# Optimization experiments

Hardware: AMD Instinct MI355X
Metric: run time of the kernel (lower is better)

Reference implementation:

```python
import jax, jax.numpy as jnp
import numpy as np

NUM_GROUPS = 32
EPS = 1e-5


def group_norm(x, scale, bias):
    # x: [B, C, H, W]
    B, C, H, W = x.shape
    g = x.reshape(B, NUM_GROUPS, C // NUM_GROUPS * H * W)
    mean = g.mean(axis=-1, keepdims=True)
    var = g.var(axis=-1, keepdims=True)
    g = (g - mean) * jax.lax.rsqrt(var + EPS)
    g = g.reshape(B, C, H, W)
    return g * scale[None, :, None, None] + bias[None, :, None, None]


def conv1x1(x, w, b):
    # x: [B, C, H, W], w: [O, C], b: [O]
    return jnp.einsum('bchw,oc->bohw', x, w) + b[None, :, None, None]


def setup_inputs() -> dict:
    key = jax.random.key(0)
    ks = jax.random.split(key, 11)
    B, C, H, W = 32, 256, 32, 32
    s = 1.0 / np.sqrt(C)
    return {
        'x': jax.random.normal(ks[0], (B, C, H, W), jnp.float32),
        'gn_scale': jnp.ones((C,), jnp.float32),
        'gn_bias': jnp.zeros((C,), jnp.float32),
        'wq': jax.random.normal(ks[1], (C, C), jnp.float32) * s,
        'bq': jnp.zeros((C,), jnp.float32),
        'wk': jax.random.normal(ks[2], (C, C), jnp.float32) * s,
        'bk': jnp.zeros((C,), jnp.float32),
        'wv': jax.random.normal(ks[3], (C, C), jnp.float32) * s,
        'bv': jnp.zeros((C,), jnp.float32),
        'wo': jax.random.normal(ks[4], (C, C), jnp.float32) * s,
        'bo': jnp.zeros((C,), jnp.float32),
    }


def reference(x, gn_scale, gn_bias, wq, bq, wk, bk, wv, bv, wo, bo):
    B, C, H, W = x.shape
    h = group_norm(x, gn_scale, gn_bias)
    q = conv1x1(h, wq, bq).reshape(B, C, H * W)  # [B, C, N]
    k = conv1x1(h, wk, bk).reshape(B, C, H * W)
    v = conv1x1(h, wv, bv).reshape(B, C, H * W)
    # scores: [B, N, N]
    w = jnp.einsum('bcn,bcm->bnm', q, k) * (C ** -0.5)
    w = jax.nn.softmax(w, axis=-1)
    o = jnp.einsum('bnm,bcm->bcn', w, v).reshape(B, C, H, W)
    o = conv1x1(o, wo, bo)
    return x + o
```

## Files before the change

kernel.cpp:

```cpp
#include <hip/hip_runtime.h>

typedef __attribute__((ext_vector_type(4))) float f32x4;
typedef __attribute__((ext_vector_type(16))) float f32x16;
typedef __attribute__((ext_vector_type(8))) short bf16x8;

__device__ __forceinline__ unsigned short f2bf(float f) {
  union { float f; unsigned u; } v; v.f = f;
  unsigned r = (v.u + 0x7FFFu + ((v.u >> 16) & 1u)) >> 16;
  return (unsigned short)r;
}

__device__ __forceinline__ unsigned cvt_pk_bf16(float lo, float hi) {
  unsigned r;
  asm("v_cvt_pk_bf16_f32 %0, %1, %2" : "=v"(r) : "v"(lo), "v"(hi));
  return r;
}

__device__ __forceinline__ void load16_lds(const void* g, void* l) {
  __builtin_amdgcn_global_load_lds(
      (__attribute__((address_space(1))) void*)(uintptr_t)g,
      (__attribute__((address_space(3))) void*)(unsigned int)(uintptr_t)l,
      16, 0, 0);
}

#define QSCALE 0.09016844f

__global__ __launch_bounds__(256) void convert_w(
    const float* __restrict__ wq, const float* __restrict__ wk,
    const float* __restrict__ wv, const float* __restrict__ wo,
    const float* __restrict__ bq, const float* __restrict__ bk,
    unsigned short* __restrict__ wqkb, unsigned short* __restrict__ wvb,
    unsigned short* __restrict__ wob, float* __restrict__ bqkf) {
  const float* src[4] = {wq, wk, wv, wo};
  unsigned short* dst[4] = {wqkb, wqkb + 65536, wvb, wob};
  int ti = blockIdx.y;
  float sc = (ti == 0) ? QSCALE : 1.f;
  int idx = blockIdx.x * 256 + threadIdx.x;
  float4 v = ((const float4*)src[ti])[idx];
  ushort4 r;
  r.x = f2bf(v.x * sc); r.y = f2bf(v.y * sc);
  r.z = f2bf(v.z * sc); r.w = f2bf(v.w * sc);
  ((ushort4*)dst[ti])[idx] = r;
  if (ti == 3 && blockIdx.x == 0) {
    bqkf[threadIdx.x] = bq[threadIdx.x] * QSCALE;
    bqkf[256 + threadIdx.x] = bk[threadIdx.x];
  }
}

__global__ __launch_bounds__(256) void gn_kernel(
    const float* __restrict__ x, const float* __restrict__ gamma,
    const float* __restrict__ beta, unsigned short* __restrict__ h) {
  __shared__ float xs[8 * 1024];
  __shared__ float red[16];
  const int t = threadIdx.x;
  const int b = blockIdx.x >> 5, g = blockIdx.x & 31;
  const float* xp = x + (size_t)(b * 256 + g * 8) * 1024;
  float s = 0.f, ss = 0.f;
#pragma unroll
  for (int j = 0; j < 8; ++j) {
    float4 v = ((const float4*)xp)[j * 256 + t];
    ((float4*)xs)[j * 256 + t] = v;
    s += v.x + v.y + v.z + v.w;
    ss += v.x * v.x + v.y * v.y + v.z * v.z + v.w * v.w;
  }
#pragma unroll
  for (int o = 32; o >= 1; o >>= 1) {
    s += __shfl_xor(s, o);
    ss += __shfl_xor(ss, o);
  }
  const int wave = t >> 6, lane = t & 63;
  if (lane == 0) { red[wave] = s; red[wave + 4] = ss; }
  __syncthreads();
  s = red[0] + red[1] + red[2] + red[3];
  ss = red[4] + red[5] + red[6] + red[7];
  float mean = s * (1.f / 8192.f);
  float var = ss * (1.f / 8192.f) - mean * mean;
  float rstd = rsqrtf(var + 1e-5f);
  float a[8], c[8];
#pragma unroll
  for (int ci = 0; ci < 8; ++ci) {
    float gm = gamma[g * 8 + ci], bt = beta[g * 8 + ci];
    a[ci] = rstd * gm;
    c[ci] = bt - mean * rstd * gm;
  }
  unsigned short* hb = h + (size_t)b * 1024 * 256 + g * 8;
#pragma unroll
  for (int j = 0; j < 4; ++j) {
    int n = j * 256 + t;
    float f0 = xs[0 * 1024 + n] * a[0] + c[0];
    float f1 = xs[1 * 1024 + n] * a[1] + c[1];
    float f2 = xs[2 * 1024 + n] * a[2] + c[2];
    float f3 = xs[3 * 1024 + n] * a[3] + c[3];
    float f4 = xs[4 * 1024 + n] * a[4] + c[4];
    float f5 = xs[5 * 1024 + n] * a[5] + c[5];
    float f6 = xs[6 * 1024 + n] * a[6] + c[6];
    float f7 = xs[7 * 1024 + n] * a[7] + c[7];
    uint4 o4;
    o4.x = (unsigned)f2bf(f0) | ((unsigned)f2bf(f1) << 16);
    o4.y = (unsigned)f2bf(f2) | ((unsigned)f2bf(f3) << 16);
    o4.z = (unsigned)f2bf(f4) | ((unsigned)f2bf(f5) << 16);
    o4.w = (unsigned)f2bf(f6) | ((unsigned)f2bf(f7) << 16);
    *(uint4*)(hb + (size_t)n * 256) = o4;
  }
}

template <bool OUT_F32, int BIAS_MODE, bool HAS_RES>
__global__ __launch_bounds__(256) void gemm_bt(
    const unsigned short* __restrict__ A, long long sAb,
    const unsigned short* __restrict__ Bm, long long sBb,
    void* __restrict__ Cv, long long sCb,
    const float* __restrict__ bias,
    const float* __restrict__ res, long long sRb,
    int M, int N, int K, float alpha) {
  __shared__ unsigned short As[128 * 32];
  __shared__ unsigned short Bs[128 * 32];
  const int t = threadIdx.x;
  const int wave = t >> 6, lane = t & 63;
  const int bm = blockIdx.y * 128, bn = blockIdx.x * 128;
  const int bz = blockIdx.z;
  const unsigned short* Ab = A + (size_t)bz * sAb;
  const unsigned short* Bb = Bm + (size_t)bz * sBb;
  const int wm = (wave >> 1) * 64, wn = (wave & 1) * 64;
  const int srow = t >> 2;
  const int schunk = t & 3;
  const int lrow = lane & 15, kg = lane >> 4;

  f32x4 acc[4][4] = {};

  for (int k0 = 0; k0 < K; k0 += 32) {
#pragma unroll
    for (int r = 0; r < 2; ++r) {
      int row = r * 64 + srow;
      int cs = schunk ^ ((row >> 1) & 3);
      const unsigned short* ga = Ab + (size_t)(bm + row) * K + (k0 + cs * 8);
      const unsigned short* gb = Bb + (size_t)(bn + row) * K + (k0 + cs * 8);
      load16_lds(ga, &As[(r * 64 + wave * 16) * 32]);
      load16_lds(gb, &Bs[(r * 64 + wave * 16) * 32]);
    }
    __syncthreads();
    bf16x8 af[4], bfr[4];
#pragma unroll
    for (int i = 0; i < 4; ++i) {
      int ra = wm + i * 16 + lrow;
      af[i] = *(const bf16x8*)&As[ra * 32 + ((kg ^ ((ra >> 1) & 3)) * 8)];
      int rb = wn + i * 16 + lrow;
      bfr[i] = *(const bf16x8*)&Bs[rb * 32 + ((kg ^ ((rb >> 1) & 3)) * 8)];
    }
#pragma unroll
    for (int i = 0; i < 4; ++i)
#pragma unroll
      for (int j = 0; j < 4; ++j)
        acc[i][j] = __builtin_amdgcn_mfma_f32_16x16x32_bf16(af[i], bfr[j], acc[i][j], 0, 0, 0);
    __syncthreads();
  }

#pragma unroll
  for (int i = 0; i < 4; ++i) {
#pragma unroll
    for (int j = 0; j < 4; ++j) {
#pragma unroll
      for (int r = 0; r < 4; ++r) {
        int m = bm + wm + i * 16 + (lane >> 4) * 4 + r;
        int n = bn + wn + j * 16 + lrow;
        float v = acc[i][j][r] * alpha;
        if constexpr (BIAS_MODE == 1) v += bias[m];
        if constexpr (BIAS_MODE == 2) v += bias[n];
        if constexpr (HAS_RES) v += res[(size_t)bz * sRb + (size_t)m * N + n];
        if constexpr (OUT_F32)
          ((float*)Cv)[(size_t)bz * sCb + (size_t)m * N + n] = v;
        else
          ((unsigned short*)Cv)[(size_t)bz * sCb + (size_t)m * N + n] = f2bf(v);
      }
    }
  }
}

__global__ __launch_bounds__(512, 2) void flash_attn(
    const unsigned short* __restrict__ qk,
    const unsigned short* __restrict__ vt,
    unsigned short* __restrict__ ot) {
  __shared__ unsigned short SMEM[81920];
  const int VS = 32768, PB = 65536;

  const int t = threadIdx.x;
  const int wave = t >> 6, lane = t & 63;
  const int wr = wave >> 1, wh = wave & 1;
  const int lrow = lane & 15, hi = lane >> 4;
  const int l31 = lane & 31, h2 = lane >> 5;

  const int lbid = blockIdx.x;
  const int logical = (lbid & 7) * 32 + (lbid >> 3);
  const int b = logical >> 3;
  const int q0 = (logical & 7) * 128;

  const unsigned short* qb = qk + (size_t)b * 1024 * 512;
  const unsigned short* kb = qb + 256;
  const unsigned short* vb = vt + (size_t)b * 1024 * 256;

#pragma unroll
  for (int p = 0; p < 4; ++p) {
    int row = p * 16 + wave * 2 + (lane >> 5);
    int ch = l31 ^ (row & 31);
    load16_lds(kb + (size_t)row * 512 + ch * 8, &SMEM[(p * 16 + wave * 2) * 256]);
  }

  bf16x8 aq[16];
#pragma unroll
  for (int kk = 0; kk < 16; ++kk)
    aq[kk] = *(const bf16x8*)(qb + (size_t)(q0 + wr * 32 + l31) * 512 + kk * 16 + h2 * 8);

  f32x4 acco[2][8] = {};
  float lsum = 0.f;

  asm volatile("s_waitcnt vmcnt(0)" ::: "memory");
  __builtin_amdgcn_s_barrier();
  __builtin_amdgcn_sched_barrier(0);

  for (int tt = 0; tt <= 16; ++tt) {
    const int cur = tt & 1, nxt = cur ^ 1;

    if (tt < 15) {
      const unsigned short* kn = kb + (size_t)(tt + 1) * 64 * 512;
#pragma unroll
      for (int p = 0; p < 4; ++p) {
        int row = p * 16 + wave * 2 + (lane >> 5);
        int ch = l31 ^ (row & 31);
        load16_lds(kn + (size_t)row * 512 + ch * 8, &SMEM[nxt * 16384 + (p * 16 + wave * 2) * 256]);
      }
    }
    if (tt < 16) {
      const unsigned short* vn = vb + tt * 64;
#pragma unroll
      for (int p = 0; p < 4; ++p) {
        int row = p * 64 + wave * 8 + (lane >> 3);
        int ch = (lane & 7) ^ (row & 7);
        load16_lds(vn + (size_t)row * 1024 + ch * 8, &SMEM[VS + cur * 16384 + (p * 64 + wave * 8) * 64]);
      }
    }

    f32x16 accs = {};
    if (tt < 16) {
      const int kbase = cur * 16384;
      const int krow = (wh * 32 + l31) * 256;
      __builtin_amdgcn_s_setprio(1);
#pragma unroll
      for (int kk = 0; kk < 16; ++kk) {
        bf16x8 kf = *(const bf16x8*)&SMEM[kbase + krow + (((kk * 2 + h2) ^ l31) << 3)];
        accs = __builtin_amdgcn_mfma_f32_32x32x16_bf16(kf, aq[kk], accs, 0, 0, 0);
      }
      __builtin_amdgcn_s_setprio(0);
    }

    if (tt >= 1) {
      const unsigned short* Pp = &SMEM[PB + nxt * 8192];
      const unsigned short* Vp = &SMEM[VS + nxt * 16384];
#pragma unroll
      for (int kk2 = 0; kk2 < 2; ++kk2) {
        int qa0 = wr * 32 + lrow;
        int qa1 = qa0 + 16;
        bf16x8 pa0 = *(const bf16x8*)&Pp[qa0 * 64 + ((kk2 * 32 + hi * 8) ^ ((qa0 & 7) << 3))];
        bf16x8 pa1 = *(const bf16x8*)&Pp[qa1 * 64 + ((kk2 * 32 + hi * 8) ^ ((qa1 & 7) << 3))];
        __builtin_amdgcn_s_setprio(1);
#pragma unroll
        for (int jj = 0; jj < 8; ++jj) {
          int c = wh * 128 + jj * 16 + lrow;
          bf16x8 bv8 = *(const bf16x8*)&Vp[c * 64 + (((kk2 * 4 + hi) ^ (c & 7)) * 8)];
          acco[0][jj] = __builtin_amdgcn_mfma_f32_16x16x32_bf16(pa0, bv8, acco[0][jj], 0, 0, 0);
          acco[1][jj] = __builtin_amdgcn_mfma_f32_16x16x32_bf16(pa1, bv8, acco[1][jj], 0, 0, 0);
        }
        __builtin_amdgcn_s_setprio(0);
      }
    }

    if (tt < 16) {
      char* Pw = (char*)&SMEM[PB + cur * 8192];
      const int q = wr * 32 + l31;
      const int qoff = q * 128 + (h2 << 3);
      const int qx = (q & 7);
#pragma unroll
      for (int m = 0; m < 4; ++m) {
        float e0 = __builtin_amdgcn_exp2f(accs[4 * m + 0]);
        float e1 = __builtin_amdgcn_exp2f(accs[4 * m + 1]);
        float e2 = __builtin_amdgcn_exp2f(accs[4 * m + 2]);
        float e3 = __builtin_amdgcn_exp2f(accs[4 * m + 3]);
        lsum += (e0 + e1) + (e2 + e3);
        uint2 w2;
        w2.x = cvt_pk_bf16(e0, e1);
        w2.y = cvt_pk_bf16(e2, e3);
        int c = wh * 4 + m;
        *(uint2*)(Pw + qoff + ((c ^ qx) << 4)) = w2;
      }
    }

    asm volatile("s_waitcnt vmcnt(0) lgkmcnt(0)" ::: "memory");
    __builtin_amdgcn_s_barrier();
    __builtin_amdgcn_sched_barrier(0);
  }

  lsum += __shfl_xor(lsum, 32);
  float* lred = (float*)SMEM;
  if (lane < 32) lred[wave * 32 + lane] = lsum;
  __syncthreads();

  unsigned short* ob = ot + (size_t)b * 1024 * 256;
#pragma unroll
  for (int i = 0; i < 2; ++i) {
    float inv[4];
#pragma unroll
    for (int r = 0; r < 4; ++r) {
      int rl = wr * 32 + i * 16 + hi * 4 + r;
      inv[r] = 1.f / (lred[wr * 64 + (rl & 31)] + lred[wr * 64 + 32 + (rl & 31)]);
    }
#pragma unroll
    for (int jj = 0; jj < 8; ++jj)
#pragma unroll
      for (int r = 0; r < 4; ++r) {
        int n = q0 + wr * 32 + i * 16 + hi * 4 + r;
        int c = wh * 128 + jj * 16 + lrow;
        ob[(size_t)n * 256 + c] = f2bf(acco[i][jj][r] * inv[r]);
      }
  }
}

extern "C" void kernel_launch(void* const* d_in, const int* in_sizes, int n_in,
                              void* d_out, int out_size, void* d_ws, size_t ws_size,
                              hipStream_t stream) {
  const float* x    = (const float*)d_in[0];
  const float* gnsc = (const float*)d_in[1];
  const float* gnb  = (const float*)d_in[2];
  const float* wq   = (const float*)d_in[3];
  const float* bq   = (const float*)d_in[4];
  const float* wk   = (const float*)d_in[5];
  const float* bk   = (const float*)d_in[6];
  const float* wv   = (const float*)d_in[7];
  const float* bv   = (const float*)d_in[8];
  const float* wo   = (const float*)d_in[9];
  const float* bo   = (const float*)d_in[10];
  float* out = (float*)d_out;

  unsigned short* wqkb = (unsigned short*)d_ws;
  unsigned short* wvb  = wqkb + 131072;
  unsigned short* wob  = wvb + 65536;
  float*          bqkf = (float*)(wob + 65536);
  unsigned short* h    = wob + 65536 + 2048;
  unsigned short* qkb  = h + 8388608;
  unsigned short* vt   = qkb + 16777216;
  unsigned short* ot   = h;

  const long long sHN = 1024LL * 256;
  const long long sQK = 1024LL * 512;

  convert_w<<<dim3(64, 4), 256, 0, stream>>>(wq, wk, wv, wo, bq, bk, wqkb, wvb, wob, bqkf);
  gn_kernel<<<dim3(1024), 256, 0, stream>>>(x, gnsc, gnb, h);
  gemm_bt<false, 2, false><<<dim3(4, 8, 32), 256, 0, stream>>>(
      h, sHN, wqkb, 0, qkb, sQK, bqkf, nullptr, 0, 1024, 512, 256, 1.f);
  gemm_bt<false, 1, false><<<dim3(8, 2, 32), 256, 0, stream>>>(
      wvb, 0, h, sHN, vt, sHN, bv, nullptr, 0, 256, 1024, 256, 1.f);
  flash_attn<<<dim3(256), 512, 0, stream>>>(qkb, vt, ot);
  gemm_bt<true, 1, true><<<dim3(8, 2, 32), 256, 0, stream>>>(
      wob, 0, ot, sHN, out, sHN, bo, x, sHN, 256, 1024, 256, 1.f);
}
```

Baseline: 118.7 us.

## Merge weight conversion into GN, fuse QK/V projections, double-buffer GEMM, reswizzle P

Folds the weight-conversion kernel into the group-norm launch as 16 extra blocks, and merges the QK and V projection GEMMs into one launch. This removes two kernel launches. The GEMM core now double-buffers its LDS tiles so the next K-slice load overlaps the MFMAs, and it raises wave priority around the MFMA block. The attention kernel's P-tile swizzle gains a row-dependent rotation to reduce LDS bank conflicts. The trade-off is twice the LDS per GEMM block and a runtime bias-mode branch in the epilogue.

Result: no change. 118.2 us (-0.4%).

```diff
diff --git a/kernel.cpp b/kernel.cpp
--- a/kernel.cpp
+++ b/kernel.cpp
@@ -25,34 +25,42 @@
 
 #define QSCALE 0.09016844f
 
-__global__ __launch_bounds__(256) void convert_w(
+__global__ __launch_bounds__(256) void gn_conv_kernel(
+    const float* __restrict__ x, const float* __restrict__ gamma,
+    const float* __restrict__ beta, unsigned short* __restrict__ h,
     const float* __restrict__ wq, const float* __restrict__ wk,
     const float* __restrict__ wv, const float* __restrict__ wo,
     const float* __restrict__ bq, const float* __restrict__ bk,
     unsigned short* __restrict__ wqkb, unsigned short* __restrict__ wvb,
     unsigned short* __restrict__ wob, float* __restrict__ bqkf) {
-  const float* src[4] = {wq, wk, wv, wo};
-  unsigned short* dst[4] = {wqkb, wqkb + 65536, wvb, wob};
-  int ti = blockIdx.y;
-  float sc = (ti == 0) ? QSCALE : 1.f;
-  int idx = blockIdx.x * 256 + threadIdx.x;
-  float4 v = ((const float4*)src[ti])[idx];
-  ushort4 r;
-  r.x = f2bf(v.x * sc); r.y = f2bf(v.y * sc);
-  r.z = f2bf(v.z * sc); r.w = f2bf(v.w * sc);
-  ((ushort4*)dst[ti])[idx] = r;
-  if (ti == 3 && blockIdx.x == 0) {
-    bqkf[threadIdx.x] = bq[threadIdx.x] * QSCALE;
-    bqkf[256 + threadIdx.x] = bk[threadIdx.x];
-  }
-}
-
-__global__ __launch_bounds__(256) void gn_kernel(
-    const float* __restrict__ x, const float* __restrict__ gamma,
-    const float* __restrict__ beta, unsigned short* __restrict__ h) {
   __shared__ float xs[8 * 1024];
   __shared__ float red[16];
   const int t = threadIdx.x;
+
+  if (blockIdx.x >= 1024) {
+    const int wblk = blockIdx.x - 1024;
+    const float* src[4] = {wq, wk, wv, wo};
+    unsigned short* dst[4] = {wqkb, wqkb + 65536, wvb, wob};
+    const int ti = wblk >> 2, part = wblk & 3;
+    const float sc = (ti == 0) ? QSCALE : 1.f;
+    const float* s = src[ti];
+    unsigned short* d = dst[ti];
+#pragma unroll
+    for (int j = 0; j < 16; ++j) {
+      int idx = part * 4096 + j * 256 + t;
+      float4 v = ((const float4*)s)[idx];
+      ushort4 r;
+      r.x = f2bf(v.x * sc); r.y = f2bf(v.y * sc);
+      r.z = f2bf(v.z * sc); r.w = f2bf(v.w * sc);
+      ((ushort4*)d)[idx] = r;
+    }
+    if (wblk == 0) {
+      bqkf[t] = bq[t] * QSCALE;
+      bqkf[256 + t] = bk[t];
+    }
+    return;
+  }
+
   const int b = blockIdx.x >> 5, g = blockIdx.x & 31;
   const float* xp = x + (size_t)(b * 256 + g * 8) * 1024;
   float s = 0.f, ss = 0.f;
@@ -104,54 +112,64 @@
   }
 }
 
-template <bool OUT_F32, int BIAS_MODE, bool HAS_RES>
-__global__ __launch_bounds__(256) void gemm_bt(
-    const unsigned short* __restrict__ A, long long sAb,
-    const unsigned short* __restrict__ Bm, long long sBb,
-    void* __restrict__ Cv, long long sCb,
-    const float* __restrict__ bias,
-    const float* __restrict__ res, long long sRb,
-    int M, int N, int K, float alpha) {
-  __shared__ unsigned short As[128 * 32];
-  __shared__ unsigned short Bs[128 * 32];
+template <bool OUT_F32, bool HAS_RES>
+__device__ __forceinline__ void gemm_core(
+    const unsigned short* __restrict__ Ab, const unsigned short* __restrict__ Bb,
+    void* __restrict__ Cb, const float* __restrict__ bias, int bias_mode,
+    const float* __restrict__ res, int bm, int bn, int N, int K,
+    unsigned short* As, unsigned short* Bs) {
   const int t = threadIdx.x;
   const int wave = t >> 6, lane = t & 63;
-  const int bm = blockIdx.y * 128, bn = blockIdx.x * 128;
-  const int bz = blockIdx.z;
-  const unsigned short* Ab = A + (size_t)bz * sAb;
-  const unsigned short* Bb = Bm + (size_t)bz * sBb;
   const int wm = (wave >> 1) * 64, wn = (wave & 1) * 64;
-  const int srow = t >> 2;
-  const int schunk = t & 3;
+  const int srow = t >> 2, schunk = t & 3;
   const int lrow = lane & 15, kg = lane >> 4;
 
   f32x4 acc[4][4] = {};
 
-  for (int k0 = 0; k0 < K; k0 += 32) {
-#pragma unroll
-    for (int r = 0; r < 2; ++r) {
-      int row = r * 64 + srow;
-      int cs = schunk ^ ((row >> 1) & 3);
-      const unsigned short* ga = Ab + (size_t)(bm + row) * K + (k0 + cs * 8);
-      const unsigned short* gb = Bb + (size_t)(bn + row) * K + (k0 + cs * 8);
-      load16_lds(ga, &As[(r * 64 + wave * 16) * 32]);
-      load16_lds(gb, &Bs[(r * 64 + wave * 16) * 32]);
-    }
-    __syncthreads();
+#pragma unroll
+  for (int r = 0; r < 2; ++r) {
+    int row = r * 64 + srow;
+    int cs = schunk ^ ((row >> 1) & 3);
+    load16_lds(Ab + (size_t)(bm + row) * K + cs * 8, &As[(r * 64 + wave * 16) * 32]);
+    load16_lds(Bb + (size_t)(bn + row) * K + cs * 8, &Bs[(r * 64 + wave * 16) * 32]);
+  }
+  asm volatile("s_waitcnt vmcnt(0)" ::: "memory");
+  __builtin_amdgcn_s_barrier();
+  __builtin_amdgcn_sched_barrier(0);
+
+  const int nk = K >> 5;
+  for (int kt = 0; kt < nk; ++kt) {
+    const int cur = kt & 1;
+    if (kt + 1 < nk) {
+      const int k0 = (kt + 1) << 5;
+      const int boff = (cur ^ 1) * 4096;
+#pragma unroll
+      for (int r = 0; r < 2; ++r) {
+        int row = r * 64 + srow;
+        int cs = schunk ^ ((row >> 1) & 3);
+        load16_lds(Ab + (size_t)(bm + row) * K + (k0 + cs * 8), &As[boff + (r * 64 + wave * 16) * 32]);
+        load16_lds(Bb + (size_t)(bn + row) * K + (k0 + cs * 8), &Bs[boff + (r * 64 + wave * 16) * 32]);
+      }
+    }
+    const int boff = cur * 4096;
     bf16x8 af[4], bfr[4];
 #pragma unroll
     for (int i = 0; i < 4; ++i) {
       int ra = wm + i * 16 + lrow;
-      af[i] = *(const bf16x8*)&As[ra * 32 + ((kg ^ ((ra >> 1) & 3)) * 8)];
+      af[i] = *(const bf16x8*)&As[boff + ra * 32 + ((kg ^ ((ra >> 1) & 3)) * 8)];
       int rb = wn + i * 16 + lrow;
-      bfr[i] = *(const bf16x8*)&Bs[rb * 32 + ((kg ^ ((rb >> 1) & 3)) * 8)];
-    }
+      bfr[i] = *(const bf16x8*)&Bs[boff + rb * 32 + ((kg ^ ((rb >> 1) & 3)) * 8)];
+    }
+    __builtin_amdgcn_s_setprio(1);
 #pragma unroll
     for (int i = 0; i < 4; ++i)
 #pragma unroll
       for (int j = 0; j < 4; ++j)
         acc[i][j] = __builtin_amdgcn_mfma_f32_16x16x32_bf16(af[i], bfr[j], acc[i][j], 0, 0, 0);
-    __syncthreads();
+    __builtin_amdgcn_s_setprio(0);
+    asm volatile("s_waitcnt vmcnt(0) lgkmcnt(0)" ::: "memory");
+    __builtin_amdgcn_s_barrier();
+    __builtin_amdgcn_sched_barrier(0);
   }
 
 #pragma unroll
@@ -160,19 +178,54 @@
     for (int j = 0; j < 4; ++j) {
 #pragma unroll
       for (int r = 0; r < 4; ++r) {
-        int m = bm + wm + i * 16 + (lane >> 4) * 4 + r;
+        int m = bm + wm + i * 16 + kg * 4 + r;
         int n = bn + wn + j * 16 + lrow;
-        float v = acc[i][j][r] * alpha;
-        if constexpr (BIAS_MODE == 1) v += bias[m];
-        if constexpr (BIAS_MODE == 2) v += bias[n];
-        if constexpr (HAS_RES) v += res[(size_t)bz * sRb + (size_t)m * N + n];
+        float v = acc[i][j][r];
+        v += (bias_mode == 1) ? bias[m] : bias[n];
+        if constexpr (HAS_RES) v += res[(size_t)m * N + n];
         if constexpr (OUT_F32)
-          ((float*)Cv)[(size_t)bz * sCb + (size_t)m * N + n] = v;
+          ((float*)Cb)[(size_t)m * N + n] = v;
         else
-          ((unsigned short*)Cv)[(size_t)bz * sCb + (size_t)m * N + n] = f2bf(v);
-      }
-    }
-  }
+          ((unsigned short*)Cb)[(size_t)m * N + n] = f2bf(v);
+      }
+    }
+  }
+}
+
+__global__ __launch_bounds__(256) void proj_kernel(
+    const unsigned short* __restrict__ h, const unsigned short* __restrict__ wqkb,
+    const unsigned short* __restrict__ wvb, unsigned short* __restrict__ qkb,
+    unsigned short* __restrict__ vtb, const float* __restrict__ bqkf,
+    const float* __restrict__ bv) {
+  __shared__ unsigned short As[2 * 4096];
+  __shared__ unsigned short Bs[2 * 4096];
+  const int tid = blockIdx.x;
+  const int bz = blockIdx.y;
+  const long long sHN = 1024LL * 256, sQK = 1024LL * 512;
+  if (tid < 32) {
+    int bn = (tid & 3) * 128, bm = (tid >> 2) * 128;
+    gemm_core<false, false>(h + bz * sHN, wqkb, qkb + bz * sQK,
+                            bqkf, 2, nullptr, bm, bn, 512, 256, As, Bs);
+  } else {
+    int t2 = tid - 32;
+    int bn = (t2 & 7) * 128, bm = (t2 >> 3) * 128;
+    gemm_core<false, false>(wvb, h + bz * sHN, vtb + bz * sHN,
+                            bv, 1, nullptr, bm, bn, 1024, 256, As, Bs);
+  }
+}
+
+__global__ __launch_bounds__(256) void out_kernel(
+    const unsigned short* __restrict__ wob, const unsigned short* __restrict__ ot,
+    float* __restrict__ out, const float* __restrict__ bo,
+    const float* __restrict__ x) {
+  __shared__ unsigned short As[2 * 4096];
+  __shared__ unsigned short Bs[2 * 4096];
+  const int tid = blockIdx.x;
+  const int bz = blockIdx.y;
+  const long long sHN = 1024LL * 256;
+  int bn = (tid & 7) * 128, bm = (tid >> 3) * 128;
+  gemm_core<true, true>(wob, ot + bz * sHN, out + bz * sHN,
+                        bo, 1, x + bz * sHN, bm, bn, 1024, 256, As, Bs);
 }
 
 __global__ __launch_bounds__(512, 2) void flash_attn(
@@ -254,12 +307,14 @@
     if (tt >= 1) {
       const unsigned short* Pp = &SMEM[PB + nxt * 8192];
       const unsigned short* Vp = &SMEM[VS + nxt * 16384];
+      const int qa0 = wr * 32 + lrow;
+      const int qa1 = qa0 + 16;
+      const int rot0 = (lrow >> 3) & 3;
+      const int rot1 = (rot0 + 2) & 3;
 #pragma unroll
       for (int kk2 = 0; kk2 < 2; ++kk2) {
-        int qa0 = wr * 32 + lrow;
-        int qa1 = qa0 + 16;
-        bf16x8 pa0 = *(const bf16x8*)&Pp[qa0 * 64 + ((kk2 * 32 + hi * 8) ^ ((qa0 & 7) << 3))];
-        bf16x8 pa1 = *(const bf16x8*)&Pp[qa1 * 64 + ((kk2 * 32 + hi * 8) ^ ((qa1 & 7) << 3))];
+        bf16x8 pa0 = *(const bf16x8*)&Pp[qa0 * 64 + ((((kk2 * 4 + hi + 2 * rot0) & 7) ^ (qa0 & 7)) << 3)];
+        bf16x8 pa1 = *(const bf16x8*)&Pp[qa1 * 64 + ((((kk2 * 4 + hi + 2 * rot1) & 7) ^ (qa1 & 7)) << 3)];
         __builtin_amdgcn_s_setprio(1);
 #pragma unroll
         for (int jj = 0; jj < 8; ++jj) {
@@ -275,8 +330,9 @@
     if (tt < 16) {
       char* Pw = (char*)&SMEM[PB + cur * 8192];
       const int q = wr * 32 + l31;
+      const int qx = q & 7;
+      const int rot2 = (l31 >> 3) & 3;
       const int qoff = q * 128 + (h2 << 3);
-      const int qx = (q & 7);
 #pragma unroll
       for (int m = 0; m < 4; ++m) {
         float e0 = __builtin_amdgcn_exp2f(accs[4 * m + 0]);
@@ -287,8 +343,8 @@
         uint2 w2;
         w2.x = cvt_pk_bf16(e0, e1);
         w2.y = cvt_pk_bf16(e2, e3);
-        int c = wh * 4 + m;
-        *(uint2*)(Pw + qoff + ((c ^ qx) << 4)) = w2;
+        int physc = ((wh * 4 + m + 2 * rot2) & 7) ^ qx;
+        *(uint2*)(Pw + qoff + (physc << 4)) = w2;
       }
     }
 
@@ -347,16 +403,9 @@
   unsigned short* vt   = qkb + 16777216;
   unsigned short* ot   = h;
 
-  const long long sHN = 1024LL * 256;
-  const long long sQK = 1024LL * 512;
-
-  convert_w<<<dim3(64, 4), 256, 0, stream>>>(wq, wk, wv, wo, bq, bk, wqkb, wvb, wob, bqkf);
-  gn_kernel<<<dim3(1024), 256, 0, stream>>>(x, gnsc, gnb, h);
-  gemm_bt<false, 2, false><<<dim3(4, 8, 32), 256, 0, stream>>>(
-      h, sHN, wqkb, 0, qkb, sQK, bqkf, nullptr, 0, 1024, 512, 256, 1.f);
-  gemm_bt<false, 1, false><<<dim3(8, 2, 32), 256, 0, stream>>>(
-      wvb, 0, h, sHN, vt, sHN, bv, nullptr, 0, 256, 1024, 256, 1.f);
+  gn_conv_kernel<<<dim3(1040), 256, 0, stream>>>(
+      x, gnsc, gnb, h, wq, wk, wv, wo, bq, bk, wqkb, wvb, wob, bqkf);
+  proj_kernel<<<dim3(48, 32), 256, 0, stream>>>(h, wqkb, wvb, qkb, vt, bqkf, bv);
   flash_attn<<<dim3(256), 512, 0, stream>>>(qkb, vt, ot);
-  gemm_bt<true, 1, true><<<dim3(8, 2, 32), 256, 0, stream>>>(
-      wob, 0, ot, sHN, out, sHN, bo, x, sHN, 256, 1024, 256, 1.f);
-}
+  out_kernel<<<dim3(16, 32), 256, 0, stream>>>(wob, ot, out, bo, x);
+}
```
